# Kernel optimization log

Measured on AMD Instinct MI355X. Metric: run time of the kernel, lower is better.

Reference implementation:

```python
import jax, jax.numpy as jnp
import numpy as np


def setup_inputs() -> dict:
    key = jax.random.key(0)
    ks = jax.random.split(key, 5)
    N, d_in, d_out, H, T = 65536, 256, 256, 8, 256
    values = jax.random.normal(ks[0], (N, d_in), jnp.float32)
    w_qkv = jax.random.normal(ks[1], (3 * d_out, d_in), jnp.float32) / np.sqrt(d_in)
    b_qkv = jax.random.normal(ks[2], (3 * d_out,), jnp.float32) * 0.01
    w_lin = jax.random.normal(ks[3], (d_out, d_out), jnp.float32) / np.sqrt(d_out)
    b_lin = jax.random.normal(ks[4], (d_out,), jnp.float32) * 0.01
    # Sorted track ids with equal-length tracks (L = N // T observations each).
    track_ids = jnp.repeat(jnp.arange(T, dtype=jnp.int32), N // T)
    return dict(values=values, w_qkv=w_qkv, b_qkv=b_qkv, w_lin=w_lin,
                b_lin=b_lin, track_ids=track_ids, n_tracks=T, num_heads=H)


def reference(values, w_qkv, b_qkv, w_lin, b_lin, track_ids, n_tracks, num_heads):
    N, d_in = values.shape
    d_out = w_qkv.shape[0] // 3
    H = num_heads
    Dh = d_out // H
    L = N // n_tracks  # static max track length (tracks are equal-length here)

    # lin_qkv over all points at once: [N, 3*d_out] -> [N, 3, H, Dh]
    qkv = (values @ w_qkv.T + b_qkv).reshape(N, 3, H, Dh)

    # Position of each point within its (sorted) track segment.
    counts = jax.ops.segment_sum(jnp.ones(N, jnp.int32), track_ids, num_segments=n_tracks)
    starts = jnp.cumsum(counts) - counts  # exclusive prefix sum
    pos = jnp.arange(N, dtype=jnp.int32) - starts[track_ids]

    # Scatter into padded per-track layout: [T, L, 3, H, Dh]
    padded = jnp.zeros((n_tracks, L, 3, H, Dh), values.dtype).at[track_ids, pos].set(qkv)
    q = jnp.transpose(padded[:, :, 0], (0, 2, 1, 3))  # [T, H, L, Dh]
    k = jnp.transpose(padded[:, :, 1], (0, 2, 1, 3))
    v = jnp.transpose(padded[:, :, 2], (0, 2, 1, 3))

    scores = jnp.einsum('thld,thmd->thlm', q, k) / np.sqrt(Dh).astype(values.dtype)
    probs = jax.nn.softmax(scores, axis=-1)
    ctx = jnp.einsum('thlm,thmd->thld', probs, v)           # [T, H, L, Dh]
    ctx = jnp.transpose(ctx, (0, 2, 1, 3)).reshape(n_tracks, L, d_out)

    # Gather back to flat point order (equals torch's track-sorted concat order).
    new_values = ctx[track_ids, pos] @ w_lin.T + b_lin      # [N, d_out]
    return new_values
```

## Files before the change

kernel.cpp:

```cpp
#include <hip/hip_runtime.h>


typedef __attribute__((ext_vector_type(8))) short short8;
typedef __attribute__((ext_vector_type(4))) float f32x4;

__device__ __forceinline__ unsigned short f2bf(float f) {
    union { float f; unsigned int i; } c; c.f = f;
    unsigned int lsb = (c.i >> 16) & 1u;
    return (unsigned short)((c.i + 0x7fffu + lsb) >> 16);
}
__device__ __forceinline__ short8 pack_bf8(f32x4 lo, f32x4 hi) {
    short8 r;
    r[0] = (short)f2bf(lo[0]); r[1] = (short)f2bf(lo[1]);
    r[2] = (short)f2bf(lo[2]); r[3] = (short)f2bf(lo[3]);
    r[4] = (short)f2bf(hi[0]); r[5] = (short)f2bf(hi[1]);
    r[6] = (short)f2bf(hi[2]); r[7] = (short)f2bf(hi[3]);
    return r;
}
__device__ __forceinline__ short8 loadB8(const unsigned short* p) { return *(const short8*)p; }
__device__ __forceinline__ short8 loadB8(const float* p) {
    return pack_bf8(*(const f32x4*)p, *(const f32x4*)(p + 4));
}

__global__ __launch_bounds__(256)
void cvt_weights(const float* __restrict__ wqkv, const float* __restrict__ wlin,
                 unsigned short* __restrict__ wb)
{
    const int i = blockIdx.x * 256 + threadIdx.x;
    const float* src = (i < 24576) ? (wqkv + (size_t)i * 8)
                                   : (wlin + (size_t)(i - 24576) * 8);
    const f32x4* p = (const f32x4*)src;
    *(short8*)(wb + (size_t)i * 8) = pack_bf8(p[0], p[1]);
}

template <typename BT>
__global__ __launch_bounds__(256)
void gemm1_k(const float* __restrict__ A, const BT* __restrict__ Bt,
             const float* __restrict__ bias, unsigned short* __restrict__ qkvb,
             float qs)
{
    __shared__ __align__(16) unsigned short As[128 * 64];
    __shared__ __align__(16) unsigned short Bs[128 * 64];
    const int tid  = threadIdx.x;
    const int lane = tid & 63;
    const int wave = tid >> 6;
    const int wm = wave >> 1, wn = wave & 1;
    const int bn = blockIdx.x, bm = blockIdx.y;
    const int fr = lane & 15, quad = lane >> 4;
    const int c8    = (tid & 7) * 8;
    const int rbase = tid >> 3;

    f32x4 zz = {0.f, 0.f, 0.f, 0.f};
    f32x4 acc[4][4];
#pragma unroll
    for (int i = 0; i < 4; ++i)
#pragma unroll
        for (int j = 0; j < 4; ++j) acc[i][j] = zz;

    for (int k0 = 0; k0 < 256; k0 += 64) {
        short8 av[4], bv[4];
#pragma unroll
        for (int i = 0; i < 4; ++i) {
            const int r = rbase + 32 * i;
            const float* ap = A + (size_t)(bm * 128 + r) * 256 + k0 + c8;
            av[i] = pack_bf8(*(const f32x4*)ap, *(const f32x4*)(ap + 4));
            bv[i] = loadB8(Bt + (size_t)(bn * 128 + r) * 256 + k0 + c8);
        }
        __syncthreads();
#pragma unroll
        for (int i = 0; i < 4; ++i) {
            const int r = rbase + 32 * i;
            *(short8*)&As[r * 64 + c8] = av[i];
            *(short8*)&Bs[r * 64 + c8] = bv[i];
        }
        __syncthreads();
#pragma unroll
        for (int kk = 0; kk < 2; ++kk) {
            short8 a[4], b[4];
            const int qa8 = (kk * 4 + quad) * 8;
#pragma unroll
            for (int f = 0; f < 4; ++f) {
                a[f] = *(const short8*)&As[(wm * 64 + f * 16 + fr) * 64 + qa8];
                b[f] = *(const short8*)&Bs[(wn * 64 + f * 16 + fr) * 64 + qa8];
            }
#pragma unroll
            for (int fm = 0; fm < 4; ++fm)
#pragma unroll
                for (int fn = 0; fn < 4; ++fn)
                    acc[fm][fn] = __builtin_amdgcn_mfma_f32_16x16x32_bf16(
                        a[fm], b[fn], acc[fm][fn], 0, 0, 0);
        }
    }
#pragma unroll
    for (int fn = 0; fn < 4; ++fn) {
        const int col = bn * 128 + wn * 64 + fn * 16 + fr;
        const int w = col >> 8, h = (col >> 5) & 7, d = col & 31;
        const float bv2 = bias[col];
        const float s = (col < 256) ? qs : 1.0f;
#pragma unroll
        for (int fm = 0; fm < 4; ++fm) {
            const int row0 = bm * 128 + wm * 64 + fm * 16 + quad * 4;
#pragma unroll
            for (int r = 0; r < 4; ++r) {
                const int row = row0 + r;
                const int t = row >> 8, l = row & 255;
                qkvb[(size_t)(((t * 8 + h) * 3 + w)) * 8192 + l * 32 + d] =
                    f2bf((acc[fm][fn][r] + bv2) * s);
            }
        }
    }
}

template <typename BT>
__global__ __launch_bounds__(256)
void gemm2_k(const unsigned short* __restrict__ qkvb, const BT* __restrict__ Bt,
             const float* __restrict__ bias, float* __restrict__ C)
{
    __shared__ __align__(16) unsigned short As[128 * 64];
    __shared__ __align__(16) unsigned short Bs[128 * 64];
    const int tid  = threadIdx.x;
    const int lane = tid & 63;
    const int wave = tid >> 6;
    const int wm = wave >> 1, wn = wave & 1;
    const int bn = blockIdx.x, bm = blockIdx.y;
    const int fr = lane & 15, quad = lane >> 4;
    const int c8    = (tid & 7) * 8;
    const int rbase = tid >> 3;
    const int t = bm >> 1;
    const int lbase = (bm & 1) * 128;

    f32x4 zz = {0.f, 0.f, 0.f, 0.f};
    f32x4 acc[4][4];
#pragma unroll
    for (int i = 0; i < 4; ++i)
#pragma unroll
        for (int j = 0; j < 4; ++j) acc[i][j] = zz;

    for (int k0 = 0; k0 < 256; k0 += 64) {
        const int kc = k0 + c8;
        const int h = kc >> 5, rem = kc & 31;
        const size_t abase = (size_t)((t * 8 + h) * 3) * 8192 + rem;
        short8 av[4], bv[4];
#pragma unroll
        for (int i = 0; i < 4; ++i) {
            const int r = rbase + 32 * i;
            av[i] = *(const short8*)(qkvb + abase + (size_t)(lbase + r) * 32);
            bv[i] = loadB8(Bt + (size_t)(bn * 128 + r) * 256 + kc);
        }
        __syncthreads();
#pragma unroll
        for (int i = 0; i < 4; ++i) {
            const int r = rbase + 32 * i;
            *(short8*)&As[r * 64 + c8] = av[i];
            *(short8*)&Bs[r * 64 + c8] = bv[i];
        }
        __syncthreads();
#pragma unroll
        for (int kk = 0; kk < 2; ++kk) {
            short8 a[4], b[4];
            const int qa8 = (kk * 4 + quad) * 8;
#pragma unroll
            for (int f = 0; f < 4; ++f) {
                a[f] = *(const short8*)&As[(wm * 64 + f * 16 + fr) * 64 + qa8];
                b[f] = *(const short8*)&Bs[(wn * 64 + f * 16 + fr) * 64 + qa8];
            }
#pragma unroll
            for (int fm = 0; fm < 4; ++fm)
#pragma unroll
                for (int fn = 0; fn < 4; ++fn)
                    acc[fm][fn] = __builtin_amdgcn_mfma_f32_16x16x32_bf16(
                        a[fm], b[fn], acc[fm][fn], 0, 0, 0);
        }
    }
#pragma unroll
    for (int fn = 0; fn < 4; ++fn) {
        const int col = bn * 128 + wn * 64 + fn * 16 + fr;
        const float bv2 = bias[col];
#pragma unroll
        for (int fm = 0; fm < 4; ++fm) {
            const int row0 = bm * 128 + wm * 64 + fm * 16 + quad * 4;
#pragma unroll
            for (int r = 0; r < 4; ++r)
                C[(size_t)(row0 + r) * 256 + col] = acc[fm][fn][r] + bv2;
        }
    }
}

__global__ __launch_bounds__(256, 4)
void attn_kernel(unsigned short* __restrict__ qkvb)
{
    __shared__ __align__(16) unsigned short vT[32 * 264];
    __shared__ __align__(16) unsigned short pbuf[4 * 2 * 64 * 20];
    const int tid = threadIdx.x, lane = tid & 63, wave = tid >> 6;
    const int t = blockIdx.x >> 3, h = blockIdx.x & 7;
    const int fr = lane & 15, quad = lane >> 4;
    const size_t baseQ = (size_t)((t * 8 + h) * 3) * 8192;
    const size_t baseK = baseQ + 8192;
    const size_t baseV = baseQ + 16384;

    {
        const unsigned short* vp = qkvb + baseV + (size_t)tid * 32;
        short8 v0 = *(const short8*)(vp);
        short8 v1 = *(const short8*)(vp + 8);
        short8 v2 = *(const short8*)(vp + 16);
        short8 v3 = *(const short8*)(vp + 24);
#pragma unroll
        for (int d = 0; d < 8; ++d) {
            vT[(d     ) * 264 + tid] = (unsigned short)v0[d];
            vT[(d +  8) * 264 + tid] = (unsigned short)v1[d];
            vT[(d + 16) * 264 + tid] = (unsigned short)v2[d];
            vT[(d + 24) * 264 + tid] = (unsigned short)v3[d];
        }
    }
    short8 qf[4];
#pragma unroll
    for (int fm = 0; fm < 4; ++fm)
        qf[fm] = *(const short8*)(qkvb + baseQ + (size_t)(wave * 64 + fm * 16 + fr) * 32 + quad * 8);

    __syncthreads();

    f32x4 zz = {0.f, 0.f, 0.f, 0.f};
    f32x4 O[4][2];
    float lsum[4][4];
#pragma unroll
    for (int fm = 0; fm < 4; ++fm) {
        O[fm][0] = zz; O[fm][1] = zz;
#pragma unroll
        for (int rg = 0; rg < 4; ++rg) lsum[fm][rg] = 0.f;
    }

    unsigned short* pw = pbuf + wave * (2 * 64 * 20);

    for (int jb = 0; jb < 4; ++jb) {
        const int j0 = jb * 64;
        short8 kf[4];
#pragma unroll
        for (int fn = 0; fn < 4; ++fn)
            kf[fn] = *(const short8*)(qkvb + baseK + (size_t)(j0 + fn * 16 + fr) * 32 + quad * 8);

        f32x4 S[4][4];
#pragma unroll
        for (int fm = 0; fm < 4; ++fm)
#pragma unroll
            for (int fn = 0; fn < 4; ++fn)
                S[fm][fn] = __builtin_amdgcn_mfma_f32_16x16x32_bf16(qf[fm], kf[fn], zz, 0, 0, 0);

#pragma unroll
        for (int kb = 0; kb < 2; ++kb) {
#pragma unroll
            for (int fm = 0; fm < 4; ++fm)
#pragma unroll
                for (int rg = 0; rg < 4; ++rg) {
                    const int prow = fm * 16 + quad * 4 + rg;
                    const float p0 = __expf(S[fm][2 * kb    ][rg]);
                    const float p1 = __expf(S[fm][2 * kb + 1][rg]);
                    lsum[fm][rg] += p0 + p1;
                    pw[          prow * 20 + fr] = f2bf(p0);
                    pw[64 * 20 + prow * 20 + fr] = f2bf(p1);
                }
            short8 pf[4], vf[2];
#pragma unroll
            for (int fm = 0; fm < 4; ++fm)
                pf[fm] = *(const short8*)&pw[(quad >> 1) * (64 * 20)
                                             + (fm * 16 + fr) * 20 + (quad & 1) * 8];
#pragma unroll
            for (int fd = 0; fd < 2; ++fd)
                vf[fd] = *(const short8*)&vT[(fd * 16 + fr) * 264 + j0 + kb * 32 + quad * 8];
#pragma unroll
            for (int fm = 0; fm < 4; ++fm)
#pragma unroll
                for (int fd = 0; fd < 2; ++fd)
                    O[fm][fd] = __builtin_amdgcn_mfma_f32_16x16x32_bf16(
                        pf[fm], vf[fd], O[fm][fd], 0, 0, 0);
        }
    }

#pragma unroll
    for (int fm = 0; fm < 4; ++fm)
#pragma unroll
        for (int rg = 0; rg < 4; ++rg) {
            float l = lsum[fm][rg];
#pragma unroll
            for (int m = 8; m >= 1; m >>= 1) l += __shfl_xor(l, m, 64);
            lsum[fm][rg] = 1.0f / l;
        }
#pragma unroll
    for (int fm = 0; fm < 4; ++fm)
#pragma unroll
        for (int fd = 0; fd < 2; ++fd)
#pragma unroll
            for (int rg = 0; rg < 4; ++rg) {
                const int row = wave * 64 + fm * 16 + quad * 4 + rg;
                const int col = fd * 16 + fr;
                qkvb[baseQ + (size_t)row * 32 + col] = f2bf(O[fm][fd][rg] * lsum[fm][rg]);
            }
}

extern "C" void kernel_launch(void* const* d_in, const int* in_sizes, int n_in,
                              void* d_out, int out_size, void* d_ws, size_t ws_size,
                              hipStream_t stream) {
    const float* values = (const float*)d_in[0];
    const float* w_qkv  = (const float*)d_in[1];
    const float* b_qkv  = (const float*)d_in[2];
    const float* w_lin  = (const float*)d_in[3];
    const float* b_lin  = (const float*)d_in[4];
    float* out = (float*)d_out;

    const float sc = 0.17677669529663687f;
    unsigned short* qkvb = (unsigned short*)d_ws;
    const size_t qkvb_elems = (size_t)65536 * 768;
    const size_t need = (qkvb_elems + 262144) * 2;

    if (ws_size >= need) {
        unsigned short* wb = qkvb + qkvb_elems;
        cvt_weights<<<dim3(128), 256, 0, stream>>>(w_qkv, w_lin, wb);
        gemm1_k<unsigned short><<<dim3(6, 512), 256, 0, stream>>>(values, wb, b_qkv, qkvb, sc);
        attn_kernel<<<dim3(2048), 256, 0, stream>>>(qkvb);
        gemm2_k<unsigned short><<<dim3(2, 512), 256, 0, stream>>>(qkvb, wb + 196608, b_lin, out);
    } else {
        gemm1_k<float><<<dim3(6, 512), 256, 0, stream>>>(values, w_qkv, b_qkv, qkvb, sc);
        attn_kernel<<<dim3(2048), 256, 0, stream>>>(qkvb);
        gemm2_k<float><<<dim3(2, 512), 256, 0, stream>>>(qkvb, w_lin, b_lin, out);
    }
}
```

Before: 295.1 us.

## Pre-convert activations to bf16 and stage GEMM tiles via direct global-to-LDS loads

Adds a pass that converts the fp32 input values to bf16 once, using the output buffer as scratch. Both GEMMs then load their A and B tiles with global_load_lds, which writes straight into shared memory instead of going through registers. Block indices are remapped so groups of 8 row tiles share column tiles, to improve L2 reuse. The cost is an extra full read/write pass over the activations, and the extra conversion launch adds latency. The in-kernel fp32-to-bf16 packing and the register round-trip are removed.

```diff
diff --git a/kernel.cpp b/kernel.cpp
--- a/kernel.cpp
+++ b/kernel.cpp
@@ -21,34 +21,50 @@
 __device__ __forceinline__ short8 loadB8(const float* p) {
     return pack_bf8(*(const f32x4*)p, *(const f32x4*)(p + 4));
 }
+__device__ __forceinline__ void glds16(const unsigned short* g, unsigned short* l) {
+    __builtin_amdgcn_global_load_lds(
+        (const __attribute__((address_space(1))) unsigned int*)g,
+        (__attribute__((address_space(3))) unsigned int*)l, 16, 0, 0);
+}
 
 __global__ __launch_bounds__(256)
-void cvt_weights(const float* __restrict__ wqkv, const float* __restrict__ wlin,
-                 unsigned short* __restrict__ wb)
+void cvt_all(const float* __restrict__ values, const float* __restrict__ wqkv,
+             const float* __restrict__ wlin, unsigned short* __restrict__ abf,
+             unsigned short* __restrict__ wb, int na8, int do_w)
 {
     const int i = blockIdx.x * 256 + threadIdx.x;
-    const float* src = (i < 24576) ? (wqkv + (size_t)i * 8)
-                                   : (wlin + (size_t)(i - 24576) * 8);
-    const f32x4* p = (const f32x4*)src;
-    *(short8*)(wb + (size_t)i * 8) = pack_bf8(p[0], p[1]);
+    if (i < na8) {
+        const f32x4* p = (const f32x4*)values + (size_t)i * 2;
+        *(short8*)(abf + (size_t)i * 8) = pack_bf8(p[0], p[1]);
+    } else if (do_w) {
+        const int j = i - na8;
+        if (j < 32768) {
+            const float* src = (j < 24576) ? wqkv + (size_t)j * 8
+                                           : wlin + (size_t)(j - 24576) * 8;
+            const f32x4* p = (const f32x4*)src;
+            *(short8*)(wb + (size_t)j * 8) = pack_bf8(p[0], p[1]);
+        }
+    }
 }
 
 template <typename BT>
 __global__ __launch_bounds__(256)
-void gemm1_k(const float* __restrict__ A, const BT* __restrict__ Bt,
+void gemm1_k(const unsigned short* __restrict__ A, const BT* __restrict__ Bt,
              const float* __restrict__ bias, unsigned short* __restrict__ qkvb,
              float qs)
 {
+    constexpr bool BF = (sizeof(BT) == 2);
     __shared__ __align__(16) unsigned short As[128 * 64];
     __shared__ __align__(16) unsigned short Bs[128 * 64];
     const int tid  = threadIdx.x;
     const int lane = tid & 63;
     const int wave = tid >> 6;
     const int wm = wave >> 1, wn = wave & 1;
-    const int bn = blockIdx.x, bm = blockIdx.y;
+    const int blk = blockIdx.x, sg = blk / 48, id = blk % 48;
+    const int bm = sg * 8 + (id & 7), bn = id >> 3;
     const int fr = lane & 15, quad = lane >> 4;
-    const int c8    = (tid & 7) * 8;
-    const int rbase = tid >> 3;
+    const int lr  = lane >> 3;
+    const int lc8 = (lane & 7) * 8;
 
     f32x4 zz = {0.f, 0.f, 0.f, 0.f};
     f32x4 acc[4][4];
@@ -57,21 +73,28 @@
 #pragma unroll
         for (int j = 0; j < 4; ++j) acc[i][j] = zz;
 
+    const unsigned short* Ab = A + (size_t)(bm * 128 + lr) * 256 + lc8;
+
     for (int k0 = 0; k0 < 256; k0 += 64) {
-        short8 av[4], bv[4];
+        short8 bv[4];
+        if constexpr (!BF) {
+#pragma unroll
+            for (int i = 0; i < 4; ++i)
+                bv[i] = loadB8(Bt + (size_t)(bn * 128 + (tid >> 3) + 32 * i) * 256 + k0 + (tid & 7) * 8);
+        }
+        __syncthreads();
 #pragma unroll
         for (int i = 0; i < 4; ++i) {
-            const int r = rbase + 32 * i;
-            const float* ap = A + (size_t)(bm * 128 + r) * 256 + k0 + c8;
-            av[i] = pack_bf8(*(const f32x4*)ap, *(const f32x4*)(ap + 4));
-            bv[i] = loadB8(Bt + (size_t)(bn * 128 + r) * 256 + k0 + c8);
-        }
-        __syncthreads();
-#pragma unroll
-        for (int i = 0; i < 4; ++i) {
-            const int r = rbase + 32 * i;
-            *(short8*)&As[r * 64 + c8] = av[i];
-            *(short8*)&Bs[r * 64 + c8] = bv[i];
+            const int r0 = i * 32 + wave * 8;
+            glds16(Ab + (size_t)r0 * 256 + k0, &As[r0 * 64]);
+            if constexpr (BF)
+                glds16((const unsigned short*)Bt + (size_t)(bn * 128 + r0 + lr) * 256 + k0 + lc8,
+                       &Bs[r0 * 64]);
+        }
+        if constexpr (!BF) {
+#pragma unroll
+            for (int i = 0; i < 4; ++i)
+                *(short8*)&Bs[((tid >> 3) + 32 * i) * 64 + (tid & 7) * 8] = bv[i];
         }
         __syncthreads();
 #pragma unroll
@@ -116,16 +139,18 @@
 void gemm2_k(const unsigned short* __restrict__ qkvb, const BT* __restrict__ Bt,
              const float* __restrict__ bias, float* __restrict__ C)
 {
+    constexpr bool BF = (sizeof(BT) == 2);
     __shared__ __align__(16) unsigned short As[128 * 64];
     __shared__ __align__(16) unsigned short Bs[128 * 64];
     const int tid  = threadIdx.x;
     const int lane = tid & 63;
     const int wave = tid >> 6;
     const int wm = wave >> 1, wn = wave & 1;
-    const int bn = blockIdx.x, bm = blockIdx.y;
+    const int blk = blockIdx.x, sg = blk / 16, id = blk % 16;
+    const int bm = sg * 8 + (id & 7), bn = id >> 3;
     const int fr = lane & 15, quad = lane >> 4;
-    const int c8    = (tid & 7) * 8;
-    const int rbase = tid >> 3;
+    const int lr  = lane >> 3;
+    const int lc8 = (lane & 7) * 8;
     const int t = bm >> 1;
     const int lbase = (bm & 1) * 128;
 
@@ -137,22 +162,29 @@
         for (int j = 0; j < 4; ++j) acc[i][j] = zz;
 
     for (int k0 = 0; k0 < 256; k0 += 64) {
-        const int kc = k0 + c8;
+        const int kc = k0 + lc8;
         const int h = kc >> 5, rem = kc & 31;
-        const size_t abase = (size_t)((t * 8 + h) * 3) * 8192 + rem;
-        short8 av[4], bv[4];
+        const unsigned short* Ab = qkvb + (size_t)((t * 8 + h) * 3) * 8192
+                                   + (size_t)(lbase + lr) * 32 + rem;
+        short8 bv[4];
+        if constexpr (!BF) {
+#pragma unroll
+            for (int i = 0; i < 4; ++i)
+                bv[i] = loadB8(Bt + (size_t)(bn * 128 + (tid >> 3) + 32 * i) * 256 + k0 + (tid & 7) * 8);
+        }
+        __syncthreads();
 #pragma unroll
         for (int i = 0; i < 4; ++i) {
-            const int r = rbase + 32 * i;
-            av[i] = *(const short8*)(qkvb + abase + (size_t)(lbase + r) * 32);
-            bv[i] = loadB8(Bt + (size_t)(bn * 128 + r) * 256 + kc);
-        }
-        __syncthreads();
-#pragma unroll
-        for (int i = 0; i < 4; ++i) {
-            const int r = rbase + 32 * i;
-            *(short8*)&As[r * 64 + c8] = av[i];
-            *(short8*)&Bs[r * 64 + c8] = bv[i];
+            const int r0 = i * 32 + wave * 8;
+            glds16(Ab + (size_t)r0 * 32, &As[r0 * 64]);
+            if constexpr (BF)
+                glds16((const unsigned short*)Bt + (size_t)(bn * 128 + r0 + lr) * 256 + k0 + lc8,
+                       &Bs[r0 * 64]);
+        }
+        if constexpr (!BF) {
+#pragma unroll
+            for (int i = 0; i < 4; ++i)
+                *(short8*)&Bs[((tid >> 3) + 32 * i) * 64 + (tid & 7) * 8] = bv[i];
         }
         __syncthreads();
 #pragma unroll
@@ -306,20 +338,24 @@
     const float* b_lin  = (const float*)d_in[4];
     float* out = (float*)d_out;
 
+    const int N = in_sizes[0] / 256;
     const float sc = 0.17677669529663687f;
     unsigned short* qkvb = (unsigned short*)d_ws;
-    const size_t qkvb_elems = (size_t)65536 * 768;
-    const size_t need = (qkvb_elems + 262144) * 2;
-
-    if (ws_size >= need) {
-        unsigned short* wb = qkvb + qkvb_elems;
-        cvt_weights<<<dim3(128), 256, 0, stream>>>(w_qkv, w_lin, wb);
-        gemm1_k<unsigned short><<<dim3(6, 512), 256, 0, stream>>>(values, wb, b_qkv, qkvb, sc);
+    const size_t qkvb_elems = (size_t)N * 768;
+    unsigned short* abf = (unsigned short*)d_out;
+    unsigned short* wb  = qkvb + qkvb_elems;
+    const int wfit = (ws_size >= (qkvb_elems + 262144) * 2) ? 1 : 0;
+    const int na8 = N * 256 / 8;
+
+    cvt_all<<<dim3((na8 + (wfit ? 32768 : 0) + 255) / 256), 256, 0, stream>>>(
+        values, w_qkv, w_lin, abf, wb, na8, wfit);
+    if (wfit) {
+        gemm1_k<unsigned short><<<dim3(3072), 256, 0, stream>>>(abf, wb, b_qkv, qkvb, sc);
         attn_kernel<<<dim3(2048), 256, 0, stream>>>(qkvb);
-        gemm2_k<unsigned short><<<dim3(2, 512), 256, 0, stream>>>(qkvb, wb + 196608, b_lin, out);
+        gemm2_k<unsigned short><<<dim3(1024), 256, 0, stream>>>(qkvb, wb + 196608, b_lin, out);
     } else {
-        gemm1_k<float><<<dim3(6, 512), 256, 0, stream>>>(values, w_qkv, b_qkv, qkvb, sc);
+        gemm1_k<float><<<dim3(3072), 256, 0, stream>>>(abf, w_qkv, b_qkv, qkvb, sc);
         attn_kernel<<<dim3(2048), 256, 0, stream>>>(qkvb);
-        gemm2_k<float><<<dim3(2, 512), 256, 0, stream>>>(qkvb, w_lin, b_lin, out);
-    }
-}
+        gemm2_k<float><<<dim3(1024), 256, 0, stream>>>(qkvb, w_lin, b_lin, out);
+    }
+}
```

Result: faster. 265.8 us (-9.9%).
